# Kernel optimization log

Measured on AMD Instinct MI355X. Metric: run time of the kernel, lower is better.

The kernel has to match this reference:

```python
import jax, jax.numpy as jnp
import numpy as np

N = 20000      # nodes
E = 320000     # edges
F = 128        # feat_dim
N_RBF = 20
CUTOFF = 5.0


def setup_inputs() -> dict:
    key = jax.random.key(0)
    ks = jax.random.split(key, 12)
    h_i = jax.random.normal(ks[0], (N, F), dtype=jnp.float32)
    v_i = jax.random.normal(ks[1], (N, F, 3), dtype=jnp.float32)
    # distances in (0, cutoff); keep strictly > 0 to avoid div-by-zero in sinc basis
    d_ij = (jax.random.uniform(ks[2], (E,), dtype=jnp.float32) * 0.98 + 0.01) * CUTOFF
    r = jax.random.normal(ks[3], (E, 3), dtype=jnp.float32)
    unit_r_ij = r / jnp.linalg.norm(r, axis=-1, keepdims=True)
    nbrs = jax.random.randint(ks[4], (E, 2), 0, N, dtype=jnp.int64)
    # params: layers = Dense(F->F, swish) then Dense(F->3F); dist_embed dense: n_rbf -> 3F
    s1 = 1.0 / np.sqrt(F)
    W1 = jax.random.uniform(ks[5], (F, F), jnp.float32, -s1, s1)
    b1 = jax.random.uniform(ks[6], (F,), jnp.float32, -s1, s1)
    W2 = jax.random.uniform(ks[7], (F, 3 * F), jnp.float32, -s1, s1)
    b2 = jax.random.uniform(ks[8], (3 * F,), jnp.float32, -s1, s1)
    sr = 1.0 / np.sqrt(N_RBF)
    Wr = jax.random.uniform(ks[9], (N_RBF, 3 * F), jnp.float32, -sr, sr)
    br = jax.random.uniform(ks[10], (3 * F,), jnp.float32, -sr, sr)
    return {"h_i": h_i, "v_i": v_i, "d_ij": d_ij, "unit_r_ij": unit_r_ij,
            "nbrs": nbrs, "W1": W1, "b1": b1, "W2": W2, "b2": b2, "Wr": Wr, "br": br}


def _dist_embed(d, Wr, br):
    # PaiNN sinc-like radial basis: sin(n*pi*d/cutoff)/d, n=1..N_RBF
    n = jnp.arange(1, N_RBF + 1, dtype=d.dtype)
    rbf = jnp.sin(n[None, :] * jnp.pi * d[:, None] / CUTOFF) / d[:, None]  # [E, N_RBF]
    # cosine cutoff envelope
    fcut = 0.5 * (jnp.cos(jnp.pi * d / CUTOFF) + 1.0) * (d < CUTOFF)       # [E]
    return (rbf @ Wr + br) * fcut[:, None]                                  # [E, 3F]


def reference(h_i, v_i, d_ij, unit_r_ij, nbrs, W1, b1, W2, b2, Wr, br):
    # phi = Dense(swish) -> Dense : [N, 3F]
    phi = jax.nn.silu(h_i @ W1 + b1) @ W2 + b2
    src = nbrs[:, 1]
    dst = nbrs[:, 0]
    edge_inv = phi[src] * _dist_embed(d_ij, Wr, br)          # [E, 3F]
    edge_inv = edge_inv.reshape(edge_inv.shape[0], 3, F)     # [E, 3, F]
    f1, f2, f3 = edge_inv[:, 0], edge_inv[:, 1], edge_inv[:, 2]
    # dv: [E, F, 3]
    dv = f1[:, :, None] * unit_r_ij[:, None, :] + f2[:, :, None] * v_i[src]
    dh_i = jax.ops.segment_sum(f3, dst, num_segments=N)      # [N, F]
    dv_i = jax.ops.segment_sum(dv, dst, num_segments=N)      # [N, F, 3]
    return (dh_i, dv_i)
```

## Files before the change

### kernel.cpp

```cpp
#include <hip/hip_runtime.h>
#include <math.h>

#define F 128
#define THREEF 384
#define N_RBF 20
#define CUTOFF 5.0f
#define CAP 64
#define TLDS_STRIDE 136

typedef __bf16 bf16x8 __attribute__((ext_vector_type(8)));
typedef float  f32x4  __attribute__((ext_vector_type(4)));
typedef float  f32x2  __attribute__((ext_vector_type(2)));
typedef _Float16 f16x2 __attribute__((ext_vector_type(2)));

static __device__ __forceinline__ float loh(unsigned int u) {
    const f16x2 h = __builtin_bit_cast(f16x2, u);
    return (float)h[0];
}
static __device__ __forceinline__ float hih(unsigned int u) {
    const f16x2 h = __builtin_bit_cast(f16x2, u);
    return (float)h[1];
}

__global__ __launch_bounds__(256) void init_kernel(
    const float* __restrict__ W1, const float* __restrict__ W2,
    const float* __restrict__ Wr,
    __bf16* __restrict__ W1T, __bf16* __restrict__ W2T,
    float* __restrict__ WrT, int* __restrict__ cnt, int N)
{
    const int tid = threadIdx.x;
    const int b   = blockIdx.x;

    if (b < 256) {
        const int idx = b * 256 + tid;
        if (idx < 128 * 128) {
            const int n = idx >> 7, k = idx & 127;
            W1T[idx] = (__bf16)W1[k * F + n];
        }
        if (idx < 384 * 128) {
            const int n = idx >> 7, k = idx & 127;
            W2T[idx] = (__bf16)W2[k * THREEF + n];
        }
    } else if (b < 264) {
        const int idx = (b - 256) * 256 + tid;
        if (idx >= 5 * 3 * 128) return;
        const int f  = idx & 127;
        const int c  = (idx >> 7) % 3;
        const int n4 = idx / (3 * 128);
        float4 v;
        v.x = Wr[(4 * n4 + 0) * THREEF + c * 128 + f];
        v.y = Wr[(4 * n4 + 1) * THREEF + c * 128 + f];
        v.z = Wr[(4 * n4 + 2) * THREEF + c * 128 + f];
        v.w = Wr[(4 * n4 + 3) * THREEF + c * 128 + f];
        ((float4*)WrT)[idx] = v;
    } else {
        const int i = (b - 264) * 256 + tid;
        if (i < (N + 3) / 4) {
            int4 z; z.x = 0; z.y = 0; z.z = 0; z.w = 0;
            ((int4*)cnt)[i] = z;
        }
    }
}

__global__ __launch_bounds__(256) void work_kernel(
    const float* __restrict__ d_ij, const float* __restrict__ unit_r,
    const int* __restrict__ nbrs, const float* __restrict__ v_i,
    int* __restrict__ cnt, float* __restrict__ pack,
    const float* __restrict__ h,
    const __bf16* __restrict__ W1T, const float* __restrict__ b1,
    const __bf16* __restrict__ W2T, const float* __restrict__ b2,
    _Float16* __restrict__ gh, int E, int EB, int MB, int N)
{
    __shared__ __bf16 t_lds[16 * TLDS_STRIDE];

    const int tid = threadIdx.x;
    const int b   = blockIdx.x;

    if (b < EB) {
        const int e = b * 256 + tid;
        if (e >= E) return;
        const int2 nb = ((const int2*)nbrs)[e];
        const int dst = nb.x;
        const int src = nb.y;
        const int slot = atomicAdd(&cnt[dst], 1);
        if (slot >= CAP) return;

        const float d = d_ij[e];
        const float x = (float)M_PI * d * (1.0f / CUTOFF);
        float sx, cx;
        __sincosf(x, &sx, &cx);
        const float fcut = (d < CUTOFF) ? 0.5f * (cx + 1.0f) : 0.0f;
        float4 q0, q1;
        q0.x = sx * fcut / d;
        q0.y = 2.0f * cx;
        q0.z = fcut;
        q0.w = unit_r[3 * e + 0];
        q1.x = unit_r[3 * e + 1];
        q1.y = unit_r[3 * e + 2];
        q1.z = __int_as_float(src);
        q1.w = 0.0f;
        float4* pk = (float4*)(pack + ((size_t)dst * CAP + slot) * 8);
        pk[0] = q0;
        pk[1] = q1;
        return;
    }

    if (b >= EB + MB) {
        const int idx = (b - EB - MB) * 256 + tid;
        if (idx >= N * F) return;
        const int node = idx >> 7, f = idx & 127;
        const float* vs = v_i + (size_t)node * THREEF + 3 * f;
        _Float16* gp = gh + (size_t)node * 768 + 6 * f + 3;
        gp[0] = (_Float16)vs[0];
        gp[1] = (_Float16)vs[1];
        gp[2] = (_Float16)vs[2];
        return;
    }

    const int wave = tid >> 6;
    const int lane = tid & 63;
    const int m    = lane & 15;
    const int quad = lane >> 4;
    const int node0 = (b - EB) * 16;
    if (node0 >= N) return;

    bf16x8 a1[4];
    #pragma unroll
    for (int kb = 0; kb < 4; ++kb) {
        const float* hp = h + (size_t)(node0 + m) * F + kb * 32 + quad * 8;
        const float4 x0 = *(const float4*)hp;
        const float4 x1 = *(const float4*)(hp + 4);
        bf16x8 a;
        a[0] = (__bf16)x0.x; a[1] = (__bf16)x0.y;
        a[2] = (__bf16)x0.z; a[3] = (__bf16)x0.w;
        a[4] = (__bf16)x1.x; a[5] = (__bf16)x1.y;
        a[6] = (__bf16)x1.z; a[7] = (__bf16)x1.w;
        a1[kb] = a;
    }

    #pragma unroll
    for (int c2 = 0; c2 < 2; ++c2) {
        const int ct = wave * 2 + c2;
        f32x4 acc = {0.0f, 0.0f, 0.0f, 0.0f};
        #pragma unroll
        for (int kb = 0; kb < 4; ++kb) {
            const bf16x8 bb =
                *(const bf16x8*)(W1T + (size_t)(ct * 16 + m) * F + kb * 32 + quad * 8);
            acc = __builtin_amdgcn_mfma_f32_16x16x32_bf16(a1[kb], bb, acc, 0, 0, 0);
        }
        const int col = ct * 16 + m;
        const float bb = b1[col];
        #pragma unroll
        for (int reg = 0; reg < 4; ++reg) {
            const float x = acc[reg] + bb;
            const float s = x / (1.0f + __expf(-x));
            t_lds[(quad * 4 + reg) * TLDS_STRIDE + col] = (__bf16)s;
        }
    }
    __syncthreads();

    bf16x8 a2[4];
    #pragma unroll
    for (int kb = 0; kb < 4; ++kb)
        a2[kb] = *(const bf16x8*)&t_lds[m * TLDS_STRIDE + kb * 32 + quad * 8];

    #pragma unroll
    for (int c6 = 0; c6 < 6; ++c6) {
        const int ct = c6 * 4 + wave;
        f32x4 acc = {0.0f, 0.0f, 0.0f, 0.0f};
        #pragma unroll
        for (int kb = 0; kb < 4; ++kb) {
            const bf16x8 bb =
                *(const bf16x8*)(W2T + (size_t)(ct * 16 + m) * F + kb * 32 + quad * 8);
            acc = __builtin_amdgcn_mfma_f32_16x16x32_bf16(a2[kb], bb, acc, 0, 0, 0);
        }
        const int col   = ct * 16 + m;
        const int plane = col >> 7;
        const int fc    = col & 127;
        const float bb  = b2[col];
        #pragma unroll
        for (int reg = 0; reg < 4; ++reg) {
            const int row = quad * 4 + reg;
            gh[(size_t)(node0 + row) * 768 + 6 * fc + plane] =
                (_Float16)(acc[reg] + bb);
        }
    }
}

__global__ __launch_bounds__(256) void gather_kernel(
    const _Float16* __restrict__ gh,
    const float* __restrict__ WrT,
    const float* __restrict__ br,
    const int*   __restrict__ cnt,
    const float* __restrict__ pack,
    float* __restrict__ dh,
    float* __restrict__ dv,
    int N)
{
    __shared__ float4 s_pack[2][CAP * 2];

    const int tid  = threadIdx.x;
    const int half = tid >> 7;
    const int f    = tid & 127;
    const int node = blockIdx.x * 2 + half;

    const int deg0 = cnt[node];
    const int deg  = deg0 < CAP ? deg0 : CAP;
    const int degR = (deg + 3) & ~3;

    {
        const float4* srcp = (const float4*)(pack + (size_t)node * CAP * 8);
        if (f < 2 * degR) {
            float4 v = make_float4(0.0f, 0.0f, 0.0f, 0.0f);
            if (f < 2 * deg) v = srcp[f];
            s_pack[half][f] = v;
        }
    }
    __syncthreads();

    const float br0 = br[f], br1 = br[f + 128], br2 = br[f + 256];
    const f32x4* wT = (const f32x4*)WrT;

    float dh_acc = 0.0f, dvx = 0.0f, dvy = 0.0f, dvz = 0.0f;

    for (int i0 = 0; i0 < degR; i0 += 4) {
        float s1[4], twoc[4], fcut[4], ux[4], uy[4], uz[4];
        float ph0[4], ph1[4], ph2[4], vx[4], vy[4], vz[4];
        #pragma unroll
        for (int j = 0; j < 4; ++j) {
            const float4 q0 = s_pack[half][2 * (i0 + j)];
            const float4 q1 = s_pack[half][2 * (i0 + j) + 1];
            s1[j] = q0.x; twoc[j] = q0.y; fcut[j] = q0.z;
            ux[j] = q0.w; uy[j] = q1.x;   uz[j] = q1.y;
            const int src = __builtin_amdgcn_readfirstlane(__float_as_int(q1.z));
            const unsigned int* gb =
                (const unsigned int*)(gh + (size_t)src * 768) + 3 * f;
            const unsigned int d0 = gb[0], d1 = gb[1], d2 = gb[2];
            ph0[j] = loh(d0); ph1[j] = hih(d0);
            ph2[j] = loh(d1); vx[j]  = hih(d1);
            vy[j]  = loh(d2); vz[j]  = hih(d2);
        }

        f32x2 t2[4], rc[4], rp[4], A0[4], A1[4], A2[4];
        #pragma unroll
        for (int j = 0; j < 4; ++j) {
            const float t2s = fmaf(twoc[j], twoc[j], -2.0f);
            t2[j][0] = t2s;      t2[j][1] = t2s;
            rc[j][0] = s1[j];    rc[j][1] = twoc[j] * s1[j];
            rp[j][0] = -s1[j];   rp[j][1] = 0.0f;
            A0[j] = (f32x2){0.0f, 0.0f};
            A1[j] = (f32x2){0.0f, 0.0f};
            A2[j] = (f32x2){0.0f, 0.0f};
        }

        #pragma unroll
        for (int n4 = 0; n4 < 5; ++n4) {
            const f32x4 w0 = wT[(n4 * 3 + 0) * 128 + f];
            const f32x4 w1 = wT[(n4 * 3 + 1) * 128 + f];
            const f32x4 w2 = wT[(n4 * 3 + 2) * 128 + f];
            const f32x2 w0lo = __builtin_shufflevector(w0, w0, 0, 1);
            const f32x2 w1lo = __builtin_shufflevector(w1, w1, 0, 1);
            const f32x2 w2lo = __builtin_shufflevector(w2, w2, 0, 1);
            const f32x2 w0hi = __builtin_shufflevector(w0, w0, 2, 3);
            const f32x2 w1hi = __builtin_shufflevector(w1, w1, 2, 3);
            const f32x2 w2hi = __builtin_shufflevector(w2, w2, 2, 3);
            #pragma unroll
            for (int j = 0; j < 4; ++j) {
                A0[j] = __builtin_elementwise_fma(rc[j], w0lo, A0[j]);
                A1[j] = __builtin_elementwise_fma(rc[j], w1lo, A1[j]);
                A2[j] = __builtin_elementwise_fma(rc[j], w2lo, A2[j]);
                f32x2 rn = __builtin_elementwise_fma(t2[j], rc[j], -rp[j]);
                rp[j] = rc[j]; rc[j] = rn;
                A0[j] = __builtin_elementwise_fma(rc[j], w0hi, A0[j]);
                A1[j] = __builtin_elementwise_fma(rc[j], w1hi, A1[j]);
                A2[j] = __builtin_elementwise_fma(rc[j], w2hi, A2[j]);
                rn = __builtin_elementwise_fma(t2[j], rc[j], -rp[j]);
                rp[j] = rc[j]; rc[j] = rn;
            }
        }

        #pragma unroll
        for (int j = 0; j < 4; ++j) {
            const float a0 = fmaf(br0, fcut[j], A0[j][0] + A0[j][1]);
            const float a1 = fmaf(br1, fcut[j], A1[j][0] + A1[j][1]);
            const float a2 = fmaf(br2, fcut[j], A2[j][0] + A2[j][1]);
            const float f1 = ph0[j] * a0;
            const float f2 = ph1[j] * a1;
            const float f3 = ph2[j] * a2;
            dh_acc += f3;
            dvx = fmaf(f1, ux[j], fmaf(f2, vx[j], dvx));
            dvy = fmaf(f1, uy[j], fmaf(f2, vy[j], dvy));
            dvz = fmaf(f1, uz[j], fmaf(f2, vz[j], dvz));
        }
    }

    dh[(size_t)node * F + f] = dh_acc;
    float* dvp = dv + (size_t)node * THREEF + 3 * f;
    dvp[0] = dvx;
    dvp[1] = dvy;
    dvp[2] = dvz;
}

extern "C" void kernel_launch(void* const* d_in, const int* in_sizes, int n_in,
                              void* d_out, int out_size, void* d_ws, size_t ws_size,
                              hipStream_t stream) {
    const float* h_i    = (const float*)d_in[0];
    const float* v_i    = (const float*)d_in[1];
    const float* d_ij   = (const float*)d_in[2];
    const float* unit_r = (const float*)d_in[3];
    const int*   nbrs   = (const int*)  d_in[4];
    const float* W1     = (const float*)d_in[5];
    const float* b1     = (const float*)d_in[6];
    const float* W2     = (const float*)d_in[7];
    const float* b2     = (const float*)d_in[8];
    const float* Wr     = (const float*)d_in[9];
    const float* br     = (const float*)d_in[10];

    const int N = in_sizes[0] / F;
    const int E = in_sizes[2];

    float* dh = (float*)d_out;
    float* dv = dh + (size_t)N * F;

    _Float16* gh = (_Float16*)d_ws;
    float* pack  = (float*)((char*)d_ws + (size_t)N * 768 * sizeof(_Float16));
    float*  WrT  = pack + (size_t)N * CAP * 8;
    int*    cnt  = (int*)(WrT + 5 * 3 * 128 * 4);
    __bf16* W1T  = (__bf16*)(cnt + N);
    __bf16* W2T  = W1T + 128 * 128;

    const int EB = (E + 255) / 256;
    const int MB = (N + 15) / 16;
    const int VB = (N * F + 255) / 256;
    const int ZB = ((N + 3) / 4 + 255) / 256;

    init_kernel<<<256 + 8 + ZB, 256, 0, stream>>>(W1, W2, Wr, W1T, W2T, WrT,
                                                  cnt, N);
    work_kernel<<<EB + MB + VB, 256, 0, stream>>>(d_ij, unit_r, nbrs, v_i,
                                                  cnt, pack, h_i, W1T, b1,
                                                  W2T, b2, gh, E, EB, MB, N);
    gather_kernel<<<N / 2, 256, 0, stream>>>(gh, WrT, br, cnt, pack,
                                             dh, dv, N);
}
```

Baseline: 278.0 us.

## Compute radial-basis embedding with bf16 MFMA per 16-edge chunk in gather kernel

The per-edge RBF-times-Wr projection was previously evaluated with scalar FMAs per feature lane. It is now computed as a 16x32 by 32x384 bf16 MFMA per chunk of 16 edges. The Chebyshev-recurrence RBF values are built once per edge into LDS, and the projected results are staged in an fp16 LDS tile. This removes redundant per-lane recurrence and FMA work. In exchange it adds block-wide syncs, pads both node halves to the larger degree in chunks of 16, and lowers precision to bf16/fp16.

Result: slower. 321.3 us (+15.6%).

```diff
diff --git a/kernel.cpp b/kernel.cpp
--- a/kernel.cpp
+++ b/kernel.cpp
@@ -7,10 +7,10 @@
 #define CUTOFF 5.0f
 #define CAP 64
 #define TLDS_STRIDE 136
+#define ASTRIDE 392
 
 typedef __bf16 bf16x8 __attribute__((ext_vector_type(8)));
 typedef float  f32x4  __attribute__((ext_vector_type(4)));
-typedef float  f32x2  __attribute__((ext_vector_type(2)));
 typedef _Float16 f16x2 __attribute__((ext_vector_type(2)));
 
 static __device__ __forceinline__ float loh(unsigned int u) {
@@ -26,7 +26,7 @@
     const float* __restrict__ W1, const float* __restrict__ W2,
     const float* __restrict__ Wr,
     __bf16* __restrict__ W1T, __bf16* __restrict__ W2T,
-    float* __restrict__ WrT, int* __restrict__ cnt, int N)
+    __bf16* __restrict__ W2C, int* __restrict__ cnt, int N)
 {
     const int tid = threadIdx.x;
     const int b   = blockIdx.x;
@@ -41,20 +41,12 @@
             const int n = idx >> 7, k = idx & 127;
             W2T[idx] = (__bf16)W2[k * THREEF + n];
         }
-    } else if (b < 264) {
+    } else if (b < 304) {
         const int idx = (b - 256) * 256 + tid;
-        if (idx >= 5 * 3 * 128) return;
-        const int f  = idx & 127;
-        const int c  = (idx >> 7) % 3;
-        const int n4 = idx / (3 * 128);
-        float4 v;
-        v.x = Wr[(4 * n4 + 0) * THREEF + c * 128 + f];
-        v.y = Wr[(4 * n4 + 1) * THREEF + c * 128 + f];
-        v.z = Wr[(4 * n4 + 2) * THREEF + c * 128 + f];
-        v.w = Wr[(4 * n4 + 3) * THREEF + c * 128 + f];
-        ((float4*)WrT)[idx] = v;
+        const int col = idx >> 5, k = idx & 31;
+        W2C[idx] = (k < N_RBF) ? (__bf16)Wr[k * THREEF + col] : (__bf16)0.0f;
     } else {
-        const int i = (b - 264) * 256 + tid;
+        const int i = (b - 304) * 256 + tid;
         if (i < (N + 3) / 4) {
             int4 z; z.x = 0; z.y = 0; z.z = 0; z.w = 0;
             ((int4*)cnt)[i] = z;
@@ -91,14 +83,14 @@
         __sincosf(x, &sx, &cx);
         const float fcut = (d < CUTOFF) ? 0.5f * (cx + 1.0f) : 0.0f;
         float4 q0, q1;
-        q0.x = sx * fcut / d;
+        q0.x = sx;
         q0.y = 2.0f * cx;
         q0.z = fcut;
         q0.w = unit_r[3 * e + 0];
         q1.x = unit_r[3 * e + 1];
         q1.y = unit_r[3 * e + 2];
         q1.z = __int_as_float(src);
-        q1.w = 0.0f;
+        q1.w = fcut / d;
         float4* pk = (float4*)(pack + ((size_t)dst * CAP + slot) * 8);
         pk[0] = q0;
         pk[1] = q1;
@@ -189,7 +181,7 @@
 
 __global__ __launch_bounds__(256) void gather_kernel(
     const _Float16* __restrict__ gh,
-    const float* __restrict__ WrT,
+    const __bf16* __restrict__ W2C,
     const float* __restrict__ br,
     const int*   __restrict__ cnt,
     const float* __restrict__ pack,
@@ -197,16 +189,29 @@
     float* __restrict__ dv,
     int N)
 {
-    __shared__ float4 s_pack[2][CAP * 2];
-
-    const int tid  = threadIdx.x;
-    const int half = tid >> 7;
-    const int f    = tid & 127;
-    const int node = blockIdx.x * 2 + half;
-
-    const int deg0 = cnt[node];
-    const int deg  = deg0 < CAP ? deg0 : CAP;
-    const int degR = (deg + 3) & ~3;
+    __shared__ float4   s_pack[2][CAP * 2];
+    __shared__ __bf16   R_lds[2][16][40];
+    __shared__ _Float16 A_lds[2][16][ASTRIDE];
+
+    const int tid   = threadIdx.x;
+    const int half  = tid >> 7;
+    const int f     = tid & 127;
+    const int wave  = tid >> 6;
+    const int lane  = tid & 63;
+    const int m     = lane & 15;
+    const int quad  = lane >> 4;
+    const int whalf = wave >> 1;
+    const int wsub  = wave & 1;
+
+    const int nb   = blockIdx.x * 2;
+    const int node = nb + half;
+
+    const int dg0 = min(cnt[nb], CAP);
+    const int dg1 = min(cnt[nb + 1], CAP);
+    const int deg = half ? dg1 : dg0;
+    const int dmax = dg0 > dg1 ? dg0 : dg1;
+    const int nchunk = (dmax + 15) >> 4;
+    const int degR = nchunk * 16;
 
     {
         const float4* srcp = (const float4*)(pack + (size_t)node * CAP * 8);
@@ -219,79 +224,66 @@
     __syncthreads();
 
     const float br0 = br[f], br1 = br[f + 128], br2 = br[f + 256];
-    const f32x4* wT = (const f32x4*)WrT;
 
     float dh_acc = 0.0f, dvx = 0.0f, dvy = 0.0f, dvz = 0.0f;
 
-    for (int i0 = 0; i0 < degR; i0 += 4) {
-        float s1[4], twoc[4], fcut[4], ux[4], uy[4], uz[4];
-        float ph0[4], ph1[4], ph2[4], vx[4], vy[4], vz[4];
-        #pragma unroll
-        for (int j = 0; j < 4; ++j) {
-            const float4 q0 = s_pack[half][2 * (i0 + j)];
-            const float4 q1 = s_pack[half][2 * (i0 + j) + 1];
-            s1[j] = q0.x; twoc[j] = q0.y; fcut[j] = q0.z;
-            ux[j] = q0.w; uy[j] = q1.x;   uz[j] = q1.y;
-            const int src = __builtin_amdgcn_readfirstlane(__float_as_int(q1.z));
+    for (int c0 = 0; c0 < degR; c0 += 16) {
+        if (f < 16) {
+            const float* q = (const float*)&s_pack[half][2 * (c0 + f)];
+            const float twoc = q[1];
+            float rp = 0.0f, rc = q[0];
+            __bf16* rr = &R_lds[half][f][0];
+            rr[0] = (__bf16)rc;
+            #pragma unroll
+            for (int n = 1; n < N_RBF; ++n) {
+                const float rn = fmaf(twoc, rc, -rp);
+                rp = rc; rc = rn;
+                rr[n] = (__bf16)rn;
+            }
+            #pragma unroll
+            for (int n = N_RBF; n < 32; ++n) rr[n] = (__bf16)0.0f;
+        }
+        __syncthreads();
+
+        const bf16x8 af = *(const bf16x8*)&R_lds[whalf][m][quad * 8];
+        #pragma unroll
+        for (int t = 0; t < 12; ++t) {
+            const int tile = wsub * 12 + t;
+            const bf16x8 bf =
+                *(const bf16x8*)(W2C + (size_t)(tile * 16 + m) * 32 + quad * 8);
+            f32x4 acc = {0.0f, 0.0f, 0.0f, 0.0f};
+            acc = __builtin_amdgcn_mfma_f32_16x16x32_bf16(af, bf, acc, 0, 0, 0);
+            const int colg = tile * 16 + m;
+            #pragma unroll
+            for (int r = 0; r < 4; ++r)
+                A_lds[whalf][quad * 4 + r][colg] = (_Float16)acc[r];
+        }
+        __syncthreads();
+
+        #pragma unroll 4
+        for (int j = 0; j < 16; ++j) {
+            const float* q = (const float*)&s_pack[half][2 * (c0 + j)];
+            const float fcut = q[2], ux = q[3], uy = q[4], uz = q[5];
+            const float scl  = q[7];
+            const int src = __builtin_amdgcn_readfirstlane(__float_as_int(q[6]));
+
+            const float a0 = fmaf(scl, (float)A_lds[half][j][f],       fcut * br0);
+            const float a1 = fmaf(scl, (float)A_lds[half][j][128 + f], fcut * br1);
+            const float a2 = fmaf(scl, (float)A_lds[half][j][256 + f], fcut * br2);
+
             const unsigned int* gb =
                 (const unsigned int*)(gh + (size_t)src * 768) + 3 * f;
             const unsigned int d0 = gb[0], d1 = gb[1], d2 = gb[2];
-            ph0[j] = loh(d0); ph1[j] = hih(d0);
-            ph2[j] = loh(d1); vx[j]  = hih(d1);
-            vy[j]  = loh(d2); vz[j]  = hih(d2);
-        }
-
-        f32x2 t2[4], rc[4], rp[4], A0[4], A1[4], A2[4];
-        #pragma unroll
-        for (int j = 0; j < 4; ++j) {
-            const float t2s = fmaf(twoc[j], twoc[j], -2.0f);
-            t2[j][0] = t2s;      t2[j][1] = t2s;
-            rc[j][0] = s1[j];    rc[j][1] = twoc[j] * s1[j];
-            rp[j][0] = -s1[j];   rp[j][1] = 0.0f;
-            A0[j] = (f32x2){0.0f, 0.0f};
-            A1[j] = (f32x2){0.0f, 0.0f};
-            A2[j] = (f32x2){0.0f, 0.0f};
-        }
-
-        #pragma unroll
-        for (int n4 = 0; n4 < 5; ++n4) {
-            const f32x4 w0 = wT[(n4 * 3 + 0) * 128 + f];
-            const f32x4 w1 = wT[(n4 * 3 + 1) * 128 + f];
-            const f32x4 w2 = wT[(n4 * 3 + 2) * 128 + f];
-            const f32x2 w0lo = __builtin_shufflevector(w0, w0, 0, 1);
-            const f32x2 w1lo = __builtin_shufflevector(w1, w1, 0, 1);
-            const f32x2 w2lo = __builtin_shufflevector(w2, w2, 0, 1);
-            const f32x2 w0hi = __builtin_shufflevector(w0, w0, 2, 3);
-            const f32x2 w1hi = __builtin_shufflevector(w1, w1, 2, 3);
-            const f32x2 w2hi = __builtin_shufflevector(w2, w2, 2, 3);
-            #pragma unroll
-            for (int j = 0; j < 4; ++j) {
-                A0[j] = __builtin_elementwise_fma(rc[j], w0lo, A0[j]);
-                A1[j] = __builtin_elementwise_fma(rc[j], w1lo, A1[j]);
-                A2[j] = __builtin_elementwise_fma(rc[j], w2lo, A2[j]);
-                f32x2 rn = __builtin_elementwise_fma(t2[j], rc[j], -rp[j]);
-                rp[j] = rc[j]; rc[j] = rn;
-                A0[j] = __builtin_elementwise_fma(rc[j], w0hi, A0[j]);
-                A1[j] = __builtin_elementwise_fma(rc[j], w1hi, A1[j]);
-                A2[j] = __builtin_elementwise_fma(rc[j], w2hi, A2[j]);
-                rn = __builtin_elementwise_fma(t2[j], rc[j], -rp[j]);
-                rp[j] = rc[j]; rc[j] = rn;
-            }
-        }
-
-        #pragma unroll
-        for (int j = 0; j < 4; ++j) {
-            const float a0 = fmaf(br0, fcut[j], A0[j][0] + A0[j][1]);
-            const float a1 = fmaf(br1, fcut[j], A1[j][0] + A1[j][1]);
-            const float a2 = fmaf(br2, fcut[j], A2[j][0] + A2[j][1]);
-            const float f1 = ph0[j] * a0;
-            const float f2 = ph1[j] * a1;
-            const float f3 = ph2[j] * a2;
+
+            const float f1 = loh(d0) * a0;
+            const float f2 = hih(d0) * a1;
+            const float f3 = loh(d1) * a2;
             dh_acc += f3;
-            dvx = fmaf(f1, ux[j], fmaf(f2, vx[j], dvx));
-            dvy = fmaf(f1, uy[j], fmaf(f2, vy[j], dvy));
-            dvz = fmaf(f1, uz[j], fmaf(f2, vz[j], dvz));
-        }
+            dvx = fmaf(f1, ux, fmaf(f2, hih(d1), dvx));
+            dvy = fmaf(f1, uy, fmaf(f2, loh(d2), dvy));
+            dvz = fmaf(f1, uz, fmaf(f2, hih(d2), dvz));
+        }
+        __syncthreads();
     }
 
     dh[(size_t)node * F + f] = dh_acc;
@@ -324,21 +316,21 @@
 
     _Float16* gh = (_Float16*)d_ws;
     float* pack  = (float*)((char*)d_ws + (size_t)N * 768 * sizeof(_Float16));
-    float*  WrT  = pack + (size_t)N * CAP * 8;
-    int*    cnt  = (int*)(WrT + 5 * 3 * 128 * 4);
+    int*    cnt  = (int*)(pack + (size_t)N * CAP * 8);
     __bf16* W1T  = (__bf16*)(cnt + N);
     __bf16* W2T  = W1T + 128 * 128;
+    __bf16* W2C  = W2T + 384 * 128;
 
     const int EB = (E + 255) / 256;
     const int MB = (N + 15) / 16;
     const int VB = (N * F + 255) / 256;
     const int ZB = ((N + 3) / 4 + 255) / 256;
 
-    init_kernel<<<256 + 8 + ZB, 256, 0, stream>>>(W1, W2, Wr, W1T, W2T, WrT,
-                                                  cnt, N);
+    init_kernel<<<304 + ZB, 256, 0, stream>>>(W1, W2, Wr, W1T, W2T, W2C,
+                                              cnt, N);
     work_kernel<<<EB + MB + VB, 256, 0, stream>>>(d_ij, unit_r, nbrs, v_i,
                                                   cnt, pack, h_i, W1T, b1,
                                                   W2T, b2, gh, E, EB, MB, N);
-    gather_kernel<<<N / 2, 256, 0, stream>>>(gh, WrT, br, cnt, pack,
+    gather_kernel<<<N / 2, 256, 0, stream>>>(gh, W2C, br, cnt, pack,
                                              dh, dv, N);
 }
```
